# Kernel optimization log

Hardware: AMD Instinct MI355X
Metric: run time of the kernel (lower is better)

## Reference

```python
import jax, jax.numpy as jnp
import numpy as np

B, C, H, W, E = 32, 64, 64, 64, 8

def setup_inputs() -> dict:
    key = jax.random.key(0)
    k1, k2, k3 = jax.random.split(key, 3)
    x = jax.random.normal(k1, (B, C, H, W), dtype=jnp.float32)
    gate_w = jax.random.normal(k2, (E, C, 3, 3), dtype=jnp.float32) * 0.02
    gate_b = jnp.zeros((E,), dtype=jnp.float32)
    expert_w = jax.random.normal(k3, (E, C, C), dtype=jnp.float32) * 0.05  # per-expert 1x1 conv (out,in)
    return {"x": x, "gate_w": gate_w, "gate_b": gate_b, "expert_w": expert_w}

def reference(x, gate_w, gate_b, expert_w):
    # Gating: Conv2d(C->E, k=3, stride=1, VALID), then sum over both spatial dims -> [B, E]
    g = jax.lax.conv_general_dilated(
        x, gate_w, window_strides=(1, 1), padding='VALID',
        dimension_numbers=('NCHW', 'OIHW', 'NCHW'))
    g = g + gate_b[None, :, None, None]
    gating_code = jnp.sum(g, axis=(2, 3))                      # [B, E]
    # softmax over experts then top-1
    probs = jax.nn.softmax(gating_code, axis=1)                # [B, E]
    top1_val = jnp.max(probs, axis=1)                          # [B]
    top1_idx = jnp.argmax(probs, axis=1)                       # [B]
    onehot = jax.nn.one_hot(top1_idx, E, dtype=x.dtype)        # [B, E]
    expert_weights = top1_val[:, None] * onehot                # combine tensor squeezed, [B, E]
    dispatch = onehot                                          # bool(combine) cast back to float == one-hot
    # einsum 'bjkd,ben->ebjkd' with n=1: broadcast x to every expert slot, masked by dispatch
    expert_inputs = x[None] * dispatch.T[:, :, None, None, None]   # [E, B, C, H, W]
    # experts: per-expert bias-free 1x1 conv (C -> C)
    expert_out = jnp.einsum('ebchw,efc->ebfhw', expert_inputs, expert_w)  # [E, B, C, H, W]
    # combine: einsum 'ij, ji... -> i...'
    output = jnp.einsum('be,ebchw->bchw', expert_weights, expert_out)      # [B, C, H, W]
    return output, expert_weights
```

## Files before the change

### kernel.cpp

```cpp
#include <hip/hip_runtime.h>

typedef float f4 __attribute__((ext_vector_type(4)));
typedef short bf16x8 __attribute__((ext_vector_type(8)));
typedef float f32x4 __attribute__((ext_vector_type(4)));

#define BB 32
#define CC 64
#define EE 8
#define HWX 4096
#define PXT 128

__device__ __forceinline__ unsigned bf16r(float f) {
  unsigned u = __builtin_bit_cast(unsigned, f);
  u += 0x7FFFu + ((u >> 16) & 1u);
  return u >> 16;
}
__device__ __forceinline__ unsigned pack2(float a, float b) {
  return bf16r(a) | (bf16r(b) << 16);
}
union frag_cast { bf16x8 v; unsigned u[4]; };

__global__ __launch_bounds__(256) void k_gate_sums(
    const float* __restrict__ x, const float* __restrict__ gate_w,
    float* __restrict__ gpart) {
  __shared__ float sg[9];
  __shared__ float cor[4][4];
  __shared__ float sS[9];
  int t = threadIdx.x;
  int bc = blockIdx.x;
  int c = bc & 63;
  const float* plane = x + (size_t)bc * HWX;
  int h = t >> 2, q = t & 3;
  const f4* rp = (const f4*)(plane + h * 64 + q * 16);
  f4 a0 = rp[0], a1 = rp[1], a2 = rp[2], a3 = rp[3];
  float local = (a0[0]+a0[1]+a0[2]+a0[3]) + (a1[0]+a1[1]+a1[2]+a1[3])
              + (a2[0]+a2[1]+a2[2]+a2[3]) + (a3[0]+a3[1]+a3[2]+a3[3]);
  if (t < 9) sg[t] = 0.f;
  __syncthreads();

  bool special = (h < 2) || (h >= 62);
  int ridx = (h < 2) ? h : h - 60;

  float red = local;
  float c0v = (q == 0) ? a0[0] : 0.f;
  float c1v = (q == 0) ? a0[1] : 0.f;
  float c2v = (q == 3) ? a3[2] : 0.f;
  float c3v = (q == 3) ? a3[3] : 0.f;
  #pragma unroll
  for (int off = 32; off > 0; off >>= 1) {
    red += __shfl_down(red, off, 64);
    c0v += __shfl_down(c0v, off, 64);
    c1v += __shfl_down(c1v, off, 64);
    c2v += __shfl_down(c2v, off, 64);
    c3v += __shfl_down(c3v, off, 64);
  }
  if ((t & 63) == 0) {
    atomicAdd(&sg[0], red);
    atomicAdd(&sg[5], c0v); atomicAdd(&sg[6], c1v);
    atomicAdd(&sg[7], c2v); atomicAdd(&sg[8], c3v);
  }

  if (special) {
    atomicAdd(&sg[1 + ridx], local);
    if (q == 0) { cor[ridx][0] = a0[0]; cor[ridx][1] = a0[1]; }
    if (q == 3) { cor[ridx][2] = a3[2]; cor[ridx][3] = a3[3]; }
  }
  __syncthreads();

  if (t == 0) {
    const int EX[3][2] = {{2,3},{0,3},{0,1}};
    float T = sg[0];
    #pragma unroll
    for (int i = 0; i < 3; i++)
      #pragma unroll
      for (int j = 0; j < 3; j++) {
        float Re = sg[1 + EX[i][0]] + sg[1 + EX[i][1]];
        float Ce = sg[5 + EX[j][0]] + sg[5 + EX[j][1]];
        float Xc = cor[EX[i][0]][EX[j][0]] + cor[EX[i][0]][EX[j][1]]
                 + cor[EX[i][1]][EX[j][0]] + cor[EX[i][1]][EX[j][1]];
        sS[i * 3 + j] = T - Re - Ce + Xc;
      }
  }
  __syncthreads();

  if (t < EE) {
    const float* gw = gate_w + ((size_t)t * CC + c) * 9;
    float ge = 0.f;
    #pragma unroll
    for (int k = 0; k < 9; k++) ge += gw[k] * sS[k];
    int b = bc >> 6;
    gpart[b * (EE * CC) + t * CC + c] = ge;
  }
}

__global__ __launch_bounds__(256) void k_mix(
    const float* __restrict__ x, const float* __restrict__ expert_w,
    const float* __restrict__ gpart, const float* __restrict__ gate_b,
    float* __restrict__ out, float* __restrict__ ew_out) {
  __shared__ float gsh[EE];
  int t = threadIdx.x;
  int pt = blockIdx.x;
  int b  = blockIdx.y;
  int wave = t >> 6;
  int lane = t & 63;
  int l15  = lane & 15;
  int quad = lane >> 4;

  const float* Xb = x + (size_t)b * CC * HWX + pt * PXT + 32 * wave;
  float xv[2][2][8];
  #pragma unroll
  for (int ss = 0; ss < 2; ss++) {
    const float* xp = Xb + ss * 16 + l15 + (size_t)(quad * 8) * HWX;
    #pragma unroll
    for (int kk = 0; kk < 2; kk++) {
      const float* xq = xp + (size_t)(kk * 32) * HWX;
      #pragma unroll
      for (int j = 0; j < 8; j++) xv[ss][kk][j] = xq[(size_t)j * HWX];
    }
  }

  {
    int e = t >> 5, j = t & 31;
    const float* gp = gpart + b * (EE * CC) + e * CC;
    float gval = gp[j] + gp[j + 32];
    #pragma unroll
    for (int off = 16; off > 0; off >>= 1) gval += __shfl_down(gval, off, 32);
    if (j == 0) gsh[e] = gval + 3844.0f * gate_b[e];
  }
  __syncthreads();

  float g[EE];
  #pragma unroll
  for (int e = 0; e < EE; e++) g[e] = gsh[e];
  int best = 0; float bg = g[0];
  #pragma unroll
  for (int e = 1; e < EE; e++) if (g[e] > bg) { bg = g[e]; best = e; }
  float s = 0.f;
  #pragma unroll
  for (int e = 0; e < EE; e++) s += __expf(g[e] - bg);
  float sc = 1.0f / s;
  if (pt == 0 && t < EE) ew_out[b * EE + t] = (t == best) ? sc : 0.f;

  const float* Wg = expert_w + (size_t)best * (CC * CC);
  bf16x8 afr[4][2];
  #pragma unroll
  for (int ft = 0; ft < 4; ft++) {
    const float* wrow = Wg + (ft * 16 + l15) * CC + quad * 8;
    #pragma unroll
    for (int kk = 0; kk < 2; kk++) {
      f4 w0 = *(const f4*)(wrow + kk * 32);
      f4 w1 = *(const f4*)(wrow + kk * 32 + 4);
      frag_cast fc;
      fc.u[0] = pack2(w0[0], w0[1]); fc.u[1] = pack2(w0[2], w0[3]);
      fc.u[2] = pack2(w1[0], w1[1]); fc.u[3] = pack2(w1[2], w1[3]);
      afr[ft][kk] = fc.v;
    }
  }

  f32x4 acc[2][4] = {};
  #pragma unroll
  for (int ss = 0; ss < 2; ss++) {
    #pragma unroll
    for (int kk = 0; kk < 2; kk++) {
      frag_cast fb;
      fb.u[0] = pack2(xv[ss][kk][0], xv[ss][kk][1]);
      fb.u[1] = pack2(xv[ss][kk][2], xv[ss][kk][3]);
      fb.u[2] = pack2(xv[ss][kk][4], xv[ss][kk][5]);
      fb.u[3] = pack2(xv[ss][kk][6], xv[ss][kk][7]);
      #pragma unroll
      for (int ft = 0; ft < 4; ft++)
        acc[ss][ft] = __builtin_amdgcn_mfma_f32_16x16x32_bf16(
            afr[ft][kk], fb.v, acc[ss][ft], 0, 0, 0);
    }
  }

  #pragma unroll
  for (int ss = 0; ss < 2; ss++) {
    #pragma unroll
    for (int ft = 0; ft < 4; ft++) {
      int f = ft * 16 + quad * 4;
      float* Og = out + ((size_t)(b * CC + f)) * HWX
                + pt * PXT + 32 * wave + ss * 16 + l15;
      #pragma unroll
      for (int r = 0; r < 4; r++)
        Og[(size_t)r * HWX] = sc * acc[ss][ft][r];
    }
  }
}

extern "C" void kernel_launch(void* const* d_in, const int* in_sizes, int n_in,
                              void* d_out, int out_size, void* d_ws, size_t ws_size,
                              hipStream_t stream) {
  const float* x        = (const float*)d_in[0];
  const float* gate_w   = (const float*)d_in[1];
  const float* gate_b   = (const float*)d_in[2];
  const float* expert_w = (const float*)d_in[3];
  float* out = (float*)d_out;
  float* ew_out = out + (size_t)BB * CC * HWX;

  float* gpart = (float*)d_ws;

  k_gate_sums<<<BB * CC, 256, 0, stream>>>(x, gate_w, gpart);
  k_mix<<<dim3(HWX / PXT, BB), 256, 0, stream>>>(x, expert_w, gpart, gate_b,
                                                 out, ew_out);
}
```

Measured before the change: 99.02 us.

## Fuse gating reduction and expert mix into one cooperative kernel with grid sync

Replaces the two-kernel pipeline with a single cooperative kernel of 512 blocks. Each block loads its slice of x into registers once, accumulates the per-channel partial sums it needs for the gate (total, edge columns, edge rows, corners), writes them to workspace, and then does a grid-wide sync. After the sync every block rebuilds the gate logits, picks the top-1 expert and runs the MFMA 1x1 conv on the x values it still holds in registers. This is meant to avoid reading x twice and to remove one kernel launch, at the cost of a grid barrier and redundant gate math in every block. If the cooperative launch fails, the code falls back to the old two-kernel path.

Measured after the change: 208.3 us. 110% more time.

```diff
diff --git a/kernel.cpp b/kernel.cpp
--- a/kernel.cpp
+++ b/kernel.cpp
@@ -1,4 +1,7 @@
 #include <hip/hip_runtime.h>
+#include <hip/hip_cooperative_groups.h>
+
+namespace cg = cooperative_groups;
 
 typedef float f4 __attribute__((ext_vector_type(4)));
 typedef short bf16x8 __attribute__((ext_vector_type(8)));
@@ -9,6 +12,7 @@
 #define EE 8
 #define HWX 4096
 #define PXT 128
+#define GPB 6400
 
 __device__ __forceinline__ unsigned bf16r(float f) {
   unsigned u = __builtin_bit_cast(unsigned, f);
@@ -19,6 +23,278 @@
   return bf16r(a) | (bf16r(b) << 16);
 }
 union frag_cast { bf16x8 v; unsigned u[4]; };
+
+__global__ __launch_bounds__(256, 2) void k_fused(
+    const float* __restrict__ x, const float* __restrict__ gate_w,
+    const float* __restrict__ gate_b, const float* __restrict__ expert_w,
+    float* __restrict__ gp, float* __restrict__ out,
+    float* __restrict__ ew_out) {
+  __shared__ float sT[CC];
+  __shared__ float sC[4 * CC];
+  __shared__ float sR[4 * CC];
+  __shared__ float sCor[16 * CC];
+  __shared__ float rT[4 * CC];
+  __shared__ float rC[16 * CC];
+  __shared__ float gsh[EE];
+
+  int t = threadIdx.x;
+  int pt = blockIdx.x;
+  int b  = blockIdx.y;
+  int wave = t >> 6, lane = t & 63, l15 = lane & 15, quad = lane >> 4;
+
+  if (t < CC) sT[t] = 0.f;
+  sC[t] = 0.f;
+  sR[t] = 0.f;
+  __syncthreads();
+
+  unsigned fbu[2][2][2][4];
+  float tpart[16];
+  #pragma unroll
+  for (int v = 0; v < 16; v++) tpart[v] = 0.f;
+
+  #pragma unroll
+  for (int tau = 0; tau < 2; tau++) {
+    const float* Xb = x + (size_t)b * CC * HWX + pt * 256 + tau * 128 + 32 * wave;
+    float xv[2][2][8];
+    #pragma unroll
+    for (int ss = 0; ss < 2; ss++) {
+      const float* xp = Xb + ss * 16 + l15 + (size_t)(quad * 8) * HWX;
+      #pragma unroll
+      for (int kk = 0; kk < 2; kk++) {
+        const float* xq = xp + (size_t)(kk * 32) * HWX;
+        #pragma unroll
+        for (int j = 0; j < 8; j++) xv[ss][kk][j] = xq[(size_t)j * HWX];
+      }
+    }
+
+    #pragma unroll
+    for (int kk = 0; kk < 2; kk++)
+      #pragma unroll
+      for (int j = 0; j < 8; j++)
+        tpart[kk * 8 + j] += xv[0][kk][j] + xv[1][kk][j];
+
+    if ((wave & 1) == 0) {
+      int cls = (l15 == 0) ? 0 : (l15 == 1) ? 1 : -1;
+      if (cls >= 0) {
+        #pragma unroll
+        for (int kk = 0; kk < 2; kk++)
+          #pragma unroll
+          for (int j = 0; j < 8; j++)
+            atomicAdd(&sC[cls * CC + quad * 8 + kk * 32 + j], xv[0][kk][j]);
+      }
+    } else {
+      int cls = (l15 == 14) ? 2 : (l15 == 15) ? 3 : -1;
+      if (cls >= 0) {
+        #pragma unroll
+        for (int kk = 0; kk < 2; kk++)
+          #pragma unroll
+          for (int j = 0; j < 8; j++)
+            atomicAdd(&sC[cls * CC + quad * 8 + kk * 32 + j], xv[1][kk][j]);
+      }
+    }
+
+    bool srow = (pt == 0 && tau == 0) || (pt == 15 && tau == 1);
+    if (srow) {
+      int slot = ((pt == 0) ? 0 : 2) + (wave >> 1);
+      float rp[16];
+      #pragma unroll
+      for (int kk = 0; kk < 2; kk++)
+        #pragma unroll
+        for (int j = 0; j < 8; j++)
+          rp[kk * 8 + j] = xv[0][kk][j] + xv[1][kk][j];
+      #pragma unroll
+      for (int off = 8; off > 0; off >>= 1)
+        #pragma unroll
+        for (int v = 0; v < 16; v++) rp[v] += __shfl_down(rp[v], off, 16);
+      if (l15 == 0) {
+        #pragma unroll
+        for (int kk = 0; kk < 2; kk++)
+          #pragma unroll
+          for (int j = 0; j < 8; j++)
+            atomicAdd(&sR[slot * CC + quad * 8 + kk * 32 + j], rp[kk * 8 + j]);
+      }
+      if ((wave & 1) == 0) {
+        int cls = (l15 == 0) ? 0 : (l15 == 1) ? 1 : -1;
+        if (cls >= 0) {
+          #pragma unroll
+          for (int kk = 0; kk < 2; kk++)
+            #pragma unroll
+            for (int j = 0; j < 8; j++)
+              sCor[(slot * 4 + cls) * CC + quad * 8 + kk * 32 + j] = xv[0][kk][j];
+        }
+      } else {
+        int cls = (l15 == 14) ? 2 : (l15 == 15) ? 3 : -1;
+        if (cls >= 0) {
+          #pragma unroll
+          for (int kk = 0; kk < 2; kk++)
+            #pragma unroll
+            for (int j = 0; j < 8; j++)
+              sCor[(slot * 4 + cls) * CC + quad * 8 + kk * 32 + j] = xv[1][kk][j];
+        }
+      }
+    }
+
+    #pragma unroll
+    for (int ss = 0; ss < 2; ss++)
+      #pragma unroll
+      for (int kk = 0; kk < 2; kk++) {
+        fbu[tau][ss][kk][0] = pack2(xv[ss][kk][0], xv[ss][kk][1]);
+        fbu[tau][ss][kk][1] = pack2(xv[ss][kk][2], xv[ss][kk][3]);
+        fbu[tau][ss][kk][2] = pack2(xv[ss][kk][4], xv[ss][kk][5]);
+        fbu[tau][ss][kk][3] = pack2(xv[ss][kk][6], xv[ss][kk][7]);
+      }
+  }
+
+  #pragma unroll
+  for (int off = 8; off > 0; off >>= 1)
+    #pragma unroll
+    for (int v = 0; v < 16; v++) tpart[v] += __shfl_down(tpart[v], off, 16);
+  if (l15 == 0) {
+    #pragma unroll
+    for (int kk = 0; kk < 2; kk++)
+      #pragma unroll
+      for (int j = 0; j < 8; j++)
+        atomicAdd(&sT[quad * 8 + kk * 32 + j], tpart[kk * 8 + j]);
+  }
+  __syncthreads();
+
+  float* gb = gp + (size_t)b * GPB;
+  if (t < CC) gb[pt * CC + t] = sT[t];
+  gb[1024 + pt * 256 + t] = sC[t];
+  if (pt == 0) {
+    if (t < 128) gb[5120 + t] = sR[t];
+    gb[5376 + t] = sCor[t];
+    gb[5376 + 256 + t] = sCor[256 + t];
+  } else if (pt == 15) {
+    if (t < 128) gb[5120 + 128 + t] = sR[128 + t];
+    gb[5376 + 512 + t] = sCor[512 + t];
+    gb[5376 + 768 + t] = sCor[768 + t];
+  }
+  __threadfence();
+
+  cg::this_grid().sync();
+
+  {
+    int ch = t & 63, grp = t >> 6;
+    float aT = 0.f, aC0 = 0.f, aC1 = 0.f, aC2 = 0.f, aC3 = 0.f;
+    #pragma unroll
+    for (int s0 = 0; s0 < 4; s0++) {
+      int s = grp * 4 + s0;
+      aT  += gb[s * CC + ch];
+      aC0 += gb[1024 + s * 256 + 0 * CC + ch];
+      aC1 += gb[1024 + s * 256 + 1 * CC + ch];
+      aC2 += gb[1024 + s * 256 + 2 * CC + ch];
+      aC3 += gb[1024 + s * 256 + 3 * CC + ch];
+    }
+    rT[grp * CC + ch] = aT;
+    rC[(grp * 4 + 0) * CC + ch] = aC0;
+    rC[(grp * 4 + 1) * CC + ch] = aC1;
+    rC[(grp * 4 + 2) * CC + ch] = aC2;
+    rC[(grp * 4 + 3) * CC + ch] = aC3;
+  }
+  __syncthreads();
+
+  if (t < CC) {
+    float T = 0.f, C[4] = {0.f, 0.f, 0.f, 0.f};
+    #pragma unroll
+    for (int g2 = 0; g2 < 4; g2++) {
+      T += rT[g2 * CC + t];
+      #pragma unroll
+      for (int c4 = 0; c4 < 4; c4++) C[c4] += rC[(g2 * 4 + c4) * CC + t];
+    }
+    float R[4], X[16];
+    #pragma unroll
+    for (int s = 0; s < 4; s++) R[s] = gb[5120 + s * CC + t];
+    #pragma unroll
+    for (int ci = 0; ci < 16; ci++) X[ci] = gb[5376 + ci * CC + t];
+    const int EX[3][2] = {{2, 3}, {0, 3}, {0, 1}};
+    float S[9];
+    #pragma unroll
+    for (int i = 0; i < 3; i++)
+      #pragma unroll
+      for (int j = 0; j < 3; j++) {
+        float Re = R[EX[i][0]] + R[EX[i][1]];
+        float Ce = C[EX[j][0]] + C[EX[j][1]];
+        float Xc = X[EX[i][0] * 4 + EX[j][0]] + X[EX[i][0] * 4 + EX[j][1]]
+                 + X[EX[i][1] * 4 + EX[j][0]] + X[EX[i][1] * 4 + EX[j][1]];
+        S[i * 3 + j] = T - Re - Ce + Xc;
+      }
+    float le[EE];
+    #pragma unroll
+    for (int e = 0; e < EE; e++) {
+      const float* gwe = gate_w + ((size_t)e * CC + t) * 9;
+      float acc = 0.f;
+      #pragma unroll
+      for (int k = 0; k < 9; k++) acc += gwe[k] * S[k];
+      le[e] = acc;
+    }
+    #pragma unroll
+    for (int off = 32; off > 0; off >>= 1)
+      #pragma unroll
+      for (int e = 0; e < EE; e++) le[e] += __shfl_down(le[e], off, 64);
+    if (t == 0) {
+      #pragma unroll
+      for (int e = 0; e < EE; e++) gsh[e] = le[e] + 3844.0f * gate_b[e];
+    }
+  }
+  __syncthreads();
+
+  float g[EE];
+  #pragma unroll
+  for (int e = 0; e < EE; e++) g[e] = gsh[e];
+  int best = 0; float bg = g[0];
+  #pragma unroll
+  for (int e = 1; e < EE; e++) if (g[e] > bg) { bg = g[e]; best = e; }
+  float s = 0.f;
+  #pragma unroll
+  for (int e = 0; e < EE; e++) s += __expf(g[e] - bg);
+  float sc = 1.0f / s;
+  if (pt == 0 && t < EE) ew_out[b * EE + t] = (t == best) ? sc : 0.f;
+
+  const float* Wg = expert_w + (size_t)best * (CC * CC);
+  bf16x8 afr[4][2];
+  #pragma unroll
+  for (int ft = 0; ft < 4; ft++) {
+    const float* wrow = Wg + (ft * 16 + l15) * CC + quad * 8;
+    #pragma unroll
+    for (int kk = 0; kk < 2; kk++) {
+      f4 w0 = *(const f4*)(wrow + kk * 32);
+      f4 w1 = *(const f4*)(wrow + kk * 32 + 4);
+      frag_cast fc;
+      fc.u[0] = pack2(w0[0], w0[1]); fc.u[1] = pack2(w0[2], w0[3]);
+      fc.u[2] = pack2(w1[0], w1[1]); fc.u[3] = pack2(w1[2], w1[3]);
+      afr[ft][kk] = fc.v;
+    }
+  }
+
+  #pragma unroll
+  for (int tau = 0; tau < 2; tau++) {
+    f32x4 acc[2][4] = {};
+    #pragma unroll
+    for (int ss = 0; ss < 2; ss++)
+      #pragma unroll
+      for (int kk = 0; kk < 2; kk++) {
+        frag_cast fb;
+        fb.u[0] = fbu[tau][ss][kk][0]; fb.u[1] = fbu[tau][ss][kk][1];
+        fb.u[2] = fbu[tau][ss][kk][2]; fb.u[3] = fbu[tau][ss][kk][3];
+        #pragma unroll
+        for (int ft = 0; ft < 4; ft++)
+          acc[ss][ft] = __builtin_amdgcn_mfma_f32_16x16x32_bf16(
+              afr[ft][kk], fb.v, acc[ss][ft], 0, 0, 0);
+      }
+    #pragma unroll
+    for (int ss = 0; ss < 2; ss++)
+      #pragma unroll
+      for (int ft = 0; ft < 4; ft++) {
+        int f = ft * 16 + quad * 4;
+        float* Og = out + ((size_t)(b * CC + f)) * HWX
+                  + pt * 256 + tau * 128 + 32 * wave + ss * 16 + l15;
+        #pragma unroll
+        for (int r = 0; r < 4; r++)
+          Og[(size_t)r * HWX] = sc * acc[ss][ft][r];
+      }
+  }
+}
 
 __global__ __launch_bounds__(256) void k_gate_sums(
     const float* __restrict__ x, const float* __restrict__ gate_w,
@@ -59,7 +335,6 @@
     atomicAdd(&sg[5], c0v); atomicAdd(&sg[6], c1v);
     atomicAdd(&sg[7], c2v); atomicAdd(&sg[8], c3v);
   }
-
   if (special) {
     atomicAdd(&sg[1 + ridx], local);
     if (q == 0) { cor[ridx][0] = a0[0]; cor[ridx][1] = a0[1]; }
@@ -197,10 +472,15 @@
   const float* expert_w = (const float*)d_in[3];
   float* out = (float*)d_out;
   float* ew_out = out + (size_t)BB * CC * HWX;
-
-  float* gpart = (float*)d_ws;
-
-  k_gate_sums<<<BB * CC, 256, 0, stream>>>(x, gate_w, gpart);
-  k_mix<<<dim3(HWX / PXT, BB), 256, 0, stream>>>(x, expert_w, gpart, gate_b,
-                                                 out, ew_out);
-}
+  float* gp = (float*)d_ws;
+
+  void* kargs[] = {(void*)&x, (void*)&gate_w, (void*)&gate_b, (void*)&expert_w,
+                   (void*)&gp, (void*)&out, (void*)&ew_out};
+  hipError_t err = hipLaunchCooperativeKernel((void*)k_fused, dim3(16, BB),
+                                              dim3(256), kargs, 0, stream);
+  if (err != hipSuccess) {
+    k_gate_sums<<<BB * CC, 256, 0, stream>>>(x, gate_w, gp);
+    k_mix<<<dim3(HWX / PXT, BB), 256, 0, stream>>>(x, expert_w, gp, gate_b,
+                                                   out, ew_out);
+  }
+}
```
